# Kernel optimization log

Hardware: AMD Instinct MI355X
Metric: run time of the kernel (lower is better)

The kernel has to match this reference:

```python
import jax, jax.numpy as jnp
import numpy as np

N = 50000      # nodes
E = 800000     # edges
F = 500        # num_features
HID = 64       # hidden_channels
H = 4          # num_heads
HC = HID // H  # headc = 16
C = 8          # num_classes
KHOP = 2       # K hops
CST = 1e-5


def setup_inputs() -> dict:
    key = jax.random.key(0)
    ks = jax.random.split(key, 12)
    s = 0.02
    return {
        "node_feat": jax.random.normal(ks[0], (N, F), dtype=jnp.float32),
        "edge_index": jax.random.randint(ks[1], (2, E), 0, N, dtype=jnp.int64),
        "Wi": jax.random.normal(ks[2], (F, HID), dtype=jnp.float32) * s,
        "bi": jnp.zeros((HID,), dtype=jnp.float32),
        "Wq": jax.random.normal(ks[3], (HID, H * HC), dtype=jnp.float32) * s,
        "bq": jnp.zeros((H * HC,), dtype=jnp.float32),
        "Wk": jax.random.normal(ks[4], (HID, H * HC), dtype=jnp.float32) * s,
        "bk": jnp.zeros((H * HC,), dtype=jnp.float32),
        "Wv": jax.random.normal(ks[5], (HID, H * C), dtype=jnp.float32) * s,
        "bv": jnp.zeros((H * C,), dtype=jnp.float32),
        "Wo": jax.random.normal(ks[6], (H * C, C), dtype=jnp.float32) * s,
        "bo": jnp.zeros((C,), dtype=jnp.float32),
        "hopwise": jnp.ones((KHOP + 1,), dtype=jnp.float32),
        "headwise": jnp.zeros((H, KHOP), dtype=jnp.float32),
        "teleport": jnp.ones((1,), dtype=jnp.float32),
    }


def reference(node_feat, edge_index, Wi, bi, Wq, bq, Wk, bk, Wv, bv, Wo, bo,
              hopwise, headwise, teleport):
    row, col = edge_index[0], edge_index[1]
    # degree(col): in-degree; norm = deg^-1 indexed at row (as in the torch code)
    deg = jax.ops.segment_sum(jnp.ones((E,), dtype=node_feat.dtype), col,
                              num_segments=N)
    deg_inv = jnp.where(deg > 0, 1.0 / deg, 0.0)  # [N]

    x = jax.nn.relu(node_feat @ Wi + bi)          # dropout p=0.0 / eval -> identity
    Q = (1.0 + jax.nn.elu(x @ Wq + bq)).reshape(N, H, HC)
    Kf = (1.0 + jax.nn.elu(x @ Wk + bk)).reshape(N, H, HC)
    V = (x @ Wv + bv).reshape(N, H, C)

    M = jnp.einsum('nhi,nhj->nhij', Kf, V)        # [N,H,HC,C]
    hidden = V * hopwise[0]                       # ind_gamma & gamma_softmax
    layerwise = jax.nn.softmax(headwise, axis=0)  # softmax over heads (dim=-2)

    # global attention (teleport) term
    teleportM = jnp.sum(M, axis=0, keepdims=True) / N      # [1,H,HC,C]
    teleportK = jnp.sum(Kf, axis=0, keepdims=True) / N     # [1,H,HC]
    teleportH = jnp.einsum('nhi,bhij->nhj', Q, teleportM)  # [N,H,C]
    teleportC = jnp.einsum('nhi,bhi->nh', Q, teleportK)[..., None] + CST
    teleportH = (teleportH / teleportC).sum(axis=-2)       # [N,C]

    for hop in range(KHOP):
        # norm[e] = deg_inv[row[e]]  =>  pre-scale source nodes, then scatter-add
        M = jax.ops.segment_sum((M * deg_inv[:, None, None, None])[row], col,
                                num_segments=N)
        Kf = jax.ops.segment_sum((Kf * deg_inv[:, None, None])[row], col,
                                 num_segments=N)
        Hh = jnp.einsum('nhi,nhij->nhj', Q, M)             # [N,H,C]
        Cc = jnp.einsum('nhi,nhi->nh', Q, Kf)[..., None] + CST
        gamma = hopwise[hop + 1] * layerwise[:, hop][:, None]  # [H,1]
        hidden = hidden + gamma * (Hh / Cc)

    # multi_concat output projection
    hidden = hidden.reshape(N, H * C) @ Wo + bo
    return hidden + teleport * teleportH
```

## Files before the change

kernel.cpp:

```cpp
#include <hip/hip_runtime.h>
#include <hip/hip_bf16.h>
#include <stdint.h>
#include <stddef.h>

#define NN 50000
#define NE 800000
#define FIN 500
#define HIDN 64
#define NH 4
#define HCD 16
#define NC 8
#define KVROW 192
#define SROW 576
#define CSTF 1e-5f
#define SCAN_NB 196
#define XBLKS 3125

typedef float f32x2 __attribute__((ext_vector_type(2)));
typedef __attribute__((ext_vector_type(8))) short bf16x8;
typedef __attribute__((ext_vector_type(4))) float f32x4;

__device__ inline float bf_lo(unsigned u) {
    union { unsigned i; float f; } v; v.i = u << 16; return v.f;
}
__device__ inline f32x2 bfpair(unsigned u) {
    union { unsigned i; float f; } lo, hi;
    lo.i = u << 16; hi.i = u & 0xffff0000u;
    f32x2 r; r.x = lo.f; r.y = hi.f; return r;
}
__device__ inline unsigned short f2bf(float f) {
    union { float f; unsigned i; } v; v.f = f;
    unsigned r = v.i + 0x7fffu + ((v.i >> 16) & 1u);
    return (unsigned short)(r >> 16);
}
__device__ inline unsigned pack2bf(float a, float b) {
    __hip_bfloat162 h = __float22bfloat162_rn(make_float2(a, b));
    unsigned r; __builtin_memcpy(&r, &h, 4); return r;
}


__global__ void k_deg_wt(const int* __restrict__ col, int* __restrict__ deg,
                         const float* __restrict__ Wi, unsigned short* __restrict__ Wt) {
    int e = blockIdx.x * blockDim.x + threadIdx.x;
    if (e < NE) atomicAdd(&deg[col[e]], 1);
    if (e < 64 * 512) {
        int c = e >> 9;
        int k = e & 511;
        Wt[e] = (k < FIN) ? f2bf(Wi[(size_t)k * 64 + c]) : (unsigned short)0;
    }
}


__global__ void k_bsum(const int* __restrict__ deg, int* __restrict__ bsum,
                       float* __restrict__ dinv, int* __restrict__ cursor,
                       float* __restrict__ tMK) {
    __shared__ int red[256];
    int b = blockIdx.x, t = threadIdx.x;
    int i = b * 256 + t;
    int d = (i < NN) ? deg[i] : 0;
    if (i < NN) {
        dinv[i] = d > 0 ? 1.0f / (float)d : 0.0f;
        cursor[i] = 0;
    }
    if (b == 0)
        for (int j = t; j < 576; j += 256) tMK[j] = 0.f;
    red[t] = d;
    __syncthreads();
    for (int s = 128; s > 0; s >>= 1) {
        if (t < s) red[t] += red[t + s];
        __syncthreads();
    }
    if (t == 0) bsum[b] = red[0];
}

__global__ void k_bscan(const int* __restrict__ bsum, int* __restrict__ bex) {
    __shared__ int s[256];
    int t = threadIdx.x;
    int own = (t < SCAN_NB) ? bsum[t] : 0;
    s[t] = own;
    __syncthreads();
    for (int d = 1; d < 256; d <<= 1) {
        int v = (t >= d) ? s[t - d] : 0;
        __syncthreads();
        s[t] += v;
        __syncthreads();
    }
    if (t < SCAN_NB) bex[t] = s[t] - own;
}

__global__ void k_expand(const int* __restrict__ deg, const int* __restrict__ bex,
                         int* __restrict__ offs) {
    __shared__ int s[256];
    int b = blockIdx.x, t = threadIdx.x;
    int i = b * 256 + t;
    int v = (i < NN) ? deg[i] : 0;
    s[t] = v;
    __syncthreads();
    for (int d = 1; d < 256; d <<= 1) {
        int a = (t >= d) ? s[t - d] : 0;
        __syncthreads();
        s[t] += a;
        __syncthreads();
    }
    int excl = s[t] - v + bex[b];
    if (i < NN) offs[i] = excl;
    if (i == NN - 1) offs[NN] = excl + v;
}

__global__ void k_scatter(const int* __restrict__ row, const int* __restrict__ col,
                          const int* __restrict__ offs, int* __restrict__ cursor,
                          int* __restrict__ csr_src) {
    int e = blockIdx.x * blockDim.x + threadIdx.x;
    if (e < NE) {
        int c = col[e];
        int pos = offs[c] + atomicAdd(&cursor[c], 1);
        csr_src[pos] = row[e];
    }
}


__global__ __launch_bounds__(256) void k_xgemm(const float* __restrict__ nf,
                                               const unsigned short* __restrict__ Wt,
                                               const float* __restrict__ bi,
                                               float* __restrict__ x) {
    __shared__ float red[4][16][68];
    int t = threadIdx.x;
    int lane = t & 63;
    int w = t >> 6;
    int quad = lane >> 4;
    int l15 = lane & 15;
    int n0 = blockIdx.x * 16;
    const float* rp = nf + (size_t)(n0 + l15) * FIN;
    int kbase = w * 128;

    float4 a0[4], a1[4];
#pragma unroll
    for (int ks = 0; ks < 4; ks++) {
        int kk = kbase + ks * 32 + quad * 8;
        int c0 = kk > 496 ? 496 : kk;
        int c1 = kk + 4 > 496 ? 496 : kk + 4;
        a0[ks] = *(const float4*)(rp + c0);
        a1[ks] = *(const float4*)(rp + c1);
    }

    f32x4 acc[4];
#pragma unroll
    for (int ct = 0; ct < 4; ct++) acc[ct] = (f32x4){0.f, 0.f, 0.f, 0.f};

#pragma unroll
    for (int ks = 0; ks < 4; ks++) {
        union { unsigned u[4]; bf16x8 v; } A;
        A.u[0] = pack2bf(a0[ks].x, a0[ks].y);
        A.u[1] = pack2bf(a0[ks].z, a0[ks].w);
        A.u[2] = pack2bf(a1[ks].x, a1[ks].y);
        A.u[3] = pack2bf(a1[ks].z, a1[ks].w);
        int kk = kbase + ks * 32 + quad * 8;
#pragma unroll
        for (int ct = 0; ct < 4; ct++) {
            bf16x8 b = *(const bf16x8*)&Wt[(size_t)(ct * 16 + l15) * 512 + kk];
            acc[ct] = __builtin_amdgcn_mfma_f32_16x16x32_bf16(A.v, b, acc[ct], 0, 0, 0);
        }
    }

#pragma unroll
    for (int ct = 0; ct < 4; ct++)
#pragma unroll
        for (int r = 0; r < 4; r++)
            red[w][quad * 4 + r][ct * 16 + l15] = acc[ct][r];
    __syncthreads();

    int ocol = t & 63;
    int orow0 = t >> 6;
    float bv = bi[ocol];
#pragma unroll
    for (int i = 0; i < 4; i++) {
        int orow = i * 4 + orow0;
        float s = red[0][orow][ocol] + red[1][orow][ocol]
                + red[2][orow][ocol] + red[3][orow][ocol];
        x[(size_t)(n0 + orow) * 64 + ocol] = fmaxf(s + bv, 0.f);
    }
}


__global__ __launch_bounds__(256) void k_qkv(const float* __restrict__ x,
    const float* __restrict__ Wq, const float* __restrict__ bq,
    const float* __restrict__ Wk, const float* __restrict__ bk,
    const float* __restrict__ Wv, const float* __restrict__ bv,
    const float* __restrict__ hopwise, const float* __restrict__ dinv,
    float* __restrict__ Qg, float* __restrict__ hid,
    unsigned char* __restrict__ kv0, float* __restrict__ tMK) {
    __shared__ float wq_s[64 * 64], wk_s[64 * 64], wv_s[64 * 32];
    __shared__ float bq_s[64], bk_s[64], bv_s[32];
    __shared__ float xs[4][8][64];
    __shared__ float tacc[576];
    int t = threadIdx.x;
    for (int i = t; i < 4096; i += 256) { wq_s[i] = Wq[i]; wk_s[i] = Wk[i]; }
    for (int i = t; i < 2048; i += 256) wv_s[i] = Wv[i];
    if (t < 64) { bq_s[t] = bq[t]; bk_s[t] = bk[t]; }
    if (t >= 64 && t < 96) bv_s[t - 64] = bv[t - 64];
    for (int i = t; i < 576; i += 256) tacc[i] = 0.f;
    __syncthreads();
    int lane = t & 63;
    int w = t >> 6;
    int h = lane >> 4;
    int vcol = lane & 31;
    float hw0 = hopwise[0];
    float tkp = 0.f;
    float tmp_[8];
#pragma unroll
    for (int j = 0; j < 8; j++) tmp_[j] = 0.f;
    int tiles = (NN + 31) >> 5;
    for (int tile = blockIdx.x; tile < tiles; tile += gridDim.x) {
        int n0 = tile * 32 + w * 8;
        __syncthreads();
#pragma unroll
        for (int u = 0; u < 8; u++) {
            int n = n0 + u;
            xs[w][u][lane] = (n < NN) ? x[(size_t)n * 64 + lane] : 0.f;
        }
        __syncthreads();
        float aq[8], ak[8], av[8];
#pragma unroll
        for (int u = 0; u < 8; u++) { aq[u] = 0.f; ak[u] = 0.f; av[u] = 0.f; }
        for (int f = 0; f < 64; f++) {
            float wqv = wq_s[f * 64 + lane];
            float wkv = wk_s[f * 64 + lane];
            float wvv = wv_s[f * 32 + vcol];
#pragma unroll
            for (int u = 0; u < 8; u++) {
                float xf = xs[w][u][f];
                aq[u] = fmaf(xf, wqv, aq[u]);
                ak[u] = fmaf(xf, wkv, ak[u]);
                av[u] = fmaf(xf, wvv, av[u]);
            }
        }
#pragma unroll
        for (int u = 0; u < 8; u++) {
            int n = n0 + u;
            float q = aq[u] + bq_s[lane];
            float k = ak[u] + bk_s[lane];
            float v = av[u] + bv_s[vcol];
            float Qv = q > 0.f ? 1.f + q : expf(q);
            float Kv = k > 0.f ? 1.f + k : expf(k);
            if (n < NN) {
                Qg[(size_t)n * 64 + lane] = Qv;
                float vj[8];
#pragma unroll
                for (int j = 0; j < 8; j++) vj[j] = __shfl(v, h * 8 + j, 64);
                tkp += Kv;
#pragma unroll
                for (int j = 0; j < 8; j++) tmp_[j] += Kv * vj[j];
                float dv = dinv[n];
                unsigned short* kvrow = (unsigned short*)(kv0 + (size_t)n * KVROW);
                kvrow[lane] = f2bf(Kv * dv);
                if (lane < 32) kvrow[64 + lane] = f2bf(v);
                if (lane < 32) hid[(size_t)n * 32 + lane] = v * hw0;
            }
        }
    }
#pragma unroll
    for (int j = 0; j < 8; j++) atomicAdd(&tacc[lane * 8 + j], tmp_[j]);
    atomicAdd(&tacc[512 + lane], tkp);
    __syncthreads();
    for (int i = t; i < 576; i += 256) atomicAdd(&tMK[i], tacc[i]);
}


__global__ __launch_bounds__(256) void k_hop0(const unsigned char* __restrict__ kv0,
    const int* __restrict__ offs, const int* __restrict__ csr_src,
    const float* __restrict__ dinv, const float* __restrict__ Qg,
    const float* __restrict__ hopwise, const float* __restrict__ headwise,
    unsigned char* __restrict__ S1, float* __restrict__ hid) {
    int t = threadIdx.x;
    int lane = t & 63;
    int n = __builtin_amdgcn_readfirstlane((blockIdx.x * 256 + t) >> 6);
    if (n >= NN) return;
    int h = lane >> 4;
    float e0 = expf(headwise[0]);
    float e1 = expf(headwise[2]);
    float e2 = expf(headwise[4]);
    float e3 = expf(headwise[6]);
    float esum = e0 + e1 + e2 + e3;
    float eh = (h == 0) ? e0 : ((h == 1) ? e1 : ((h == 2) ? e2 : e3));
    float gam = hopwise[1] * eh / esum;

    int hoff = 128 + h * 16;
    int o0 = offs[n], o1 = offs[n + 1];
    float qv = Qg[(size_t)n * 64 + lane];
    float kacc = 0.f;
    f32x2 A0 = {0.f, 0.f}, A1 = {0.f, 0.f}, B0 = {0.f, 0.f}, B1 = {0.f, 0.f};

    int idx[8];
#pragma unroll
    for (int q = 0; q < 8; q++) idx[q] = (o0 + q < o1) ? csr_src[o0 + q] : NN;
    for (int e = o0; e < o1; e += 8) {
        float kk_[8]; uint4 vv[8];
#pragma unroll
        for (int q = 0; q < 8; q++) {
            const unsigned char* r = kv0 + (size_t)idx[q] * KVROW;
            kk_[q] = bf_lo(((const unsigned short*)r)[lane]);
            vv[q] = *(const uint4*)(r + hoff);
        }
        int e2n = e + 8;
#pragma unroll
        for (int q = 0; q < 8; q++) idx[q] = (e2n + q < o1) ? csr_src[e2n + q] : NN;
#pragma unroll
        for (int q = 0; q < 8; q++) {
            float ka = kk_[q];
            f32x2 ka2; ka2.x = ka; ka2.y = ka;
            kacc += ka;
            A0 += ka2 * bfpair(vv[q].x);
            A1 += ka2 * bfpair(vv[q].y);
            B0 += ka2 * bfpair(vv[q].z);
            B1 += ka2 * bfpair(vv[q].w);
        }
    }
    {
        float dv = dinv[n];
        float s8 = dv * 8.f;
        float s16 = dv * 16.f;
        unsigned char* drow = S1 + (size_t)n * SROW;
        unsigned kb8 = __builtin_amdgcn_cvt_pk_fp8_f32(kacc * s8, 0.f, 0, false);
        drow[lane] = (unsigned char)(kb8 & 0xff);
        unsigned u0 = __builtin_amdgcn_cvt_pk_fp8_f32(A0.x * s16, A0.y * s16, 0, false);
        u0 = __builtin_amdgcn_cvt_pk_fp8_f32(A1.x * s16, A1.y * s16, u0, true);
        unsigned u1 = __builtin_amdgcn_cvt_pk_fp8_f32(B0.x * s16, B0.y * s16, 0, false);
        u1 = __builtin_amdgcn_cvt_pk_fp8_f32(B1.x * s16, B1.y * s16, u1, true);
        uint2 pv; pv.x = u0; pv.y = u1;
        *(uint2*)(drow + 64 + lane * 8) = pv;
    }
    float hh[8];
    hh[0] = qv * A0.x; hh[1] = qv * A0.y; hh[2] = qv * A1.x; hh[3] = qv * A1.y;
    hh[4] = qv * B0.x; hh[5] = qv * B0.y; hh[6] = qv * B1.x; hh[7] = qv * B1.y;
    float cc = qv * kacc;
#pragma unroll
    for (int s = 1; s < 16; s <<= 1) {
#pragma unroll
        for (int j = 0; j < 8; j++) hh[j] += __shfl_xor(hh[j], s, 16);
        cc += __shfl_xor(cc, s, 16);
    }
    if ((lane & 15) < 8) {
        int j = lane & 7;
        float val = j < 4 ? (j < 2 ? (j == 0 ? hh[0] : hh[1]) : (j == 2 ? hh[2] : hh[3]))
                          : (j < 6 ? (j == 4 ? hh[4] : hh[5]) : (j == 6 ? hh[6] : hh[7]));
        size_t idx2 = (size_t)n * 32 + h * 8 + j;
        hid[idx2] += gam * val / (cc + CSTF);
    }
}


__global__ __launch_bounds__(256) void k_prop1(const unsigned char* __restrict__ Sold,
    const int* __restrict__ offs, const int* __restrict__ csr_src,
    const float* __restrict__ Qg, const float* __restrict__ hopwise,
    const float* __restrict__ headwise, float* __restrict__ hid) {
    int t = threadIdx.x;
    int lane = t & 63;
    int n = __builtin_amdgcn_readfirstlane((blockIdx.x * 256 + t) >> 6);
    if (n >= NN) return;
    int h = lane >> 4;
    float e0 = expf(headwise[1]);
    float e1 = expf(headwise[3]);
    float e2 = expf(headwise[5]);
    float e3 = expf(headwise[7]);
    float esum = e0 + e1 + e2 + e3;
    float eh = (h == 0) ? e0 : ((h == 1) ? e1 : ((h == 2) ? e2 : e3));
    float gam = hopwise[2] * eh / esum * 0.0625f;

    int o0 = offs[n], o1 = offs[n + 1];
    float qv = Qg[(size_t)n * 64 + lane];
    float kacc = 0.f;
    f32x2 A0 = {0.f, 0.f}, A1 = {0.f, 0.f}, B0 = {0.f, 0.f}, B1 = {0.f, 0.f};

    int idx[8];
#pragma unroll
    for (int q = 0; q < 8; q++) idx[q] = (o0 + q < o1) ? csr_src[o0 + q] : NN;
    for (int e = o0; e < o1; e += 8) {
        unsigned kb[8]; uint2 mv[8];
#pragma unroll
        for (int q = 0; q < 8; q++) {
            const unsigned char* r = Sold + (size_t)idx[q] * SROW;
            kb[q] = r[lane];
            mv[q] = *(const uint2*)(r + 64 + lane * 8);
        }
        int e2n = e + 8;
#pragma unroll
        for (int q = 0; q < 8; q++) idx[q] = (e2n + q < o1) ? csr_src[e2n + q] : NN;
#pragma unroll
        for (int q = 0; q < 8; q++) {
            f32x2 kv = __builtin_amdgcn_cvt_pk_f32_fp8(kb[q], false);
            kacc += kv.x;
            A0 += __builtin_amdgcn_cvt_pk_f32_fp8(mv[q].x, false);
            A1 += __builtin_amdgcn_cvt_pk_f32_fp8(mv[q].x, true);
            B0 += __builtin_amdgcn_cvt_pk_f32_fp8(mv[q].y, false);
            B1 += __builtin_amdgcn_cvt_pk_f32_fp8(mv[q].y, true);
        }
    }
    kacc *= 0.125f;
    float hh[8];
    hh[0] = qv * A0.x; hh[1] = qv * A0.y; hh[2] = qv * A1.x; hh[3] = qv * A1.y;
    hh[4] = qv * B0.x; hh[5] = qv * B0.y; hh[6] = qv * B1.x; hh[7] = qv * B1.y;
    float cc = qv * kacc;
#pragma unroll
    for (int s = 1; s < 16; s <<= 1) {
#pragma unroll
        for (int j = 0; j < 8; j++) hh[j] += __shfl_xor(hh[j], s, 16);
        cc += __shfl_xor(cc, s, 16);
    }
    if ((lane & 15) < 8) {
        int j = lane & 7;
        float val = j < 4 ? (j < 2 ? (j == 0 ? hh[0] : hh[1]) : (j == 2 ? hh[2] : hh[3]))
                          : (j < 6 ? (j == 4 ? hh[4] : hh[5]) : (j == 6 ? hh[6] : hh[7]));
        size_t idx2 = (size_t)n * 32 + h * 8 + j;
        hid[idx2] += gam * val / (cc + CSTF);
    }
}


__global__ __launch_bounds__(256) void k_final(const float* __restrict__ hid,
    const float* __restrict__ Qg, const float* __restrict__ Wo,
    const float* __restrict__ bo, const float* __restrict__ tMK,
    const float* __restrict__ teleport, float* __restrict__ out) {
    __shared__ float tm[512];
    __shared__ float tk[64];
    __shared__ float wo[256];
    __shared__ float bos[8];
    int t = threadIdx.x;
    const float invN = 1.0f / (float)NN;
    for (int i = t; i < 512; i += 256) tm[i] = tMK[i] * invN;
    if (t < 64) tk[t] = tMK[512 + t] * invN;
    wo[t] = Wo[t & 255];
    if (t < 8) bos[t] = bo[t];
    __syncthreads();
    float tp = teleport[0];
    int lane = t & 63;
    int sub = lane & 7;
    int g = lane >> 3;
    int wid = (blockIdx.x * 256 + t) >> 6;
    int nwaves = gridDim.x * 4;
    for (int nb = wid * 8; nb < NN; nb += nwaves * 8) {
        int n = nb + g;
        if (n < NN) {
            const float* hrow = hid + (size_t)n * 32;
            const float* qrow = Qg + (size_t)n * 64;
            float o = bos[sub];
#pragma unroll
            for (int m = 0; m < 32; m++) o = fmaf(hrow[m], wo[m * 8 + sub], o);
            float th = 0.f;
#pragma unroll
            for (int h2 = 0; h2 < 4; h2++) {
                float num = 0.f, den = 0.f;
#pragma unroll
                for (int i = 0; i < 16; i++) {
                    float q = qrow[h2 * 16 + i];
                    num = fmaf(q, tm[h2 * 128 + i * 8 + sub], num);
                    den = fmaf(q, tk[h2 * 16 + i], den);
                }
                th += num / (den + CSTF);
            }
            out[(size_t)n * 8 + sub] = o + tp * th;
        }
    }
}


extern "C" void kernel_launch(void* const* d_in, const int* in_sizes, int n_in,
                              void* d_out, int out_size, void* d_ws, size_t ws_size,
                              hipStream_t stream) {
    const float* nf = (const float*)d_in[0];
    const int* ei = (const int*)d_in[1];
    const float* Wi = (const float*)d_in[2];
    const float* bi = (const float*)d_in[3];
    const float* Wq = (const float*)d_in[4];
    const float* bq = (const float*)d_in[5];
    const float* Wk = (const float*)d_in[6];
    const float* bk = (const float*)d_in[7];
    const float* Wv = (const float*)d_in[8];
    const float* bv = (const float*)d_in[9];
    const float* Wo = (const float*)d_in[10];
    const float* bo = (const float*)d_in[11];
    const float* hopwise = (const float*)d_in[12];
    const float* headwise = (const float*)d_in[13];
    const float* teleport = (const float*)d_in[14];
    float* out = (float*)d_out;

    char* base = (char*)d_ws;
    size_t off = 0;
    auto alloc = [&](size_t bytes) -> void* {
        void* p = base + off;
        off = (off + bytes + 255) & ~(size_t)255;
        return p;
    };
    int* deg = (int*)alloc(NN * 4);
    int* cursor = (int*)alloc(NN * 4);
    int* offs = (int*)alloc((NN + 1) * 4);
    int* bsum = (int*)alloc(256 * 4);
    int* bex = (int*)alloc(256 * 4);
    float* dinv = (float*)alloc(NN * 4);
    int* csr_src = (int*)alloc((size_t)NE * 4);
    unsigned short* Wt = (unsigned short*)alloc(64 * 512 * 2);
    float* xbuf = (float*)alloc((size_t)NN * 64 * 4);
    float* Qg = (float*)alloc((size_t)NN * 64 * 4);
    float* hid = (float*)alloc((size_t)NN * 32 * 4);
    unsigned char* kv0 = (unsigned char*)alloc((size_t)(NN + 1) * KVROW);
    unsigned char* S1 = (unsigned char*)alloc((size_t)(NN + 1) * SROW);
    float* tMK = (float*)alloc(576 * 4);

    const int* rowp = ei;
    const int* colp = ei + NE;

    hipMemsetAsync(deg, 0, NN * 4, stream);
    hipMemsetAsync(kv0 + (size_t)NN * KVROW, 0, KVROW, stream);
    hipMemsetAsync(S1 + (size_t)NN * SROW, 0, SROW, stream);

    k_deg_wt<<<(NE + 255) / 256, 256, 0, stream>>>(colp, deg, Wi, Wt);
    k_bsum<<<SCAN_NB, 256, 0, stream>>>(deg, bsum, dinv, cursor, tMK);
    k_bscan<<<1, 256, 0, stream>>>(bsum, bex);
    k_expand<<<SCAN_NB, 256, 0, stream>>>(deg, bex, offs);
    k_scatter<<<(NE + 255) / 256, 256, 0, stream>>>(rowp, colp, offs, cursor, csr_src);
    k_xgemm<<<XBLKS, 256, 0, stream>>>(nf, Wt, bi, xbuf);
    k_qkv<<<768, 256, 0, stream>>>(xbuf, Wq, bq, Wk, bk, Wv, bv, hopwise, dinv,
                                   Qg, hid, kv0, tMK);
    k_hop0<<<(NN * 64 + 255) / 256, 256, 0, stream>>>(kv0, offs, csr_src, dinv, Qg,
                                                      hopwise, headwise, S1, hid);
    k_prop1<<<(NN * 64 + 255) / 256, 256, 0, stream>>>(S1, offs, csr_src, Qg,
                                                       hopwise, headwise, hid);
    k_final<<<1563, 256, 0, stream>>>(hid, Qg, Wo, bo, tMK, teleport, out);
}
```

Measured before the change: 458.4 us.

## Split wave into half-waves per edge and realign propagated K/M arrays

Both hop kernels now process two neighbours per wave iteration, one per half-wave. Each lane owns two K channels and accumulates the full 2x8 KV outer-product slice for them, and the two halves are combined with a cross-half shuffle. The single 576-byte fp8 S1 row is replaced by separate 512-byte M and 64-byte K arrays, and the kv0 row stride is padded from 192 to 256 bytes. This gives aligned 16-byte loads and stores and halves the number of gather instructions per edge. The cost is extra shuffles and a padded kv0 buffer.

```diff
diff --git a/kernel.cpp b/kernel.cpp
--- a/kernel.cpp
+++ b/kernel.cpp
@@ -10,8 +10,7 @@
 #define NH 4
 #define HCD 16
 #define NC 8
-#define KVROW 192
-#define SROW 576
+#define KVROW 256
 #define CSTF 1e-5f
 #define SCAN_NB 196
 #define XBLKS 3125
@@ -270,12 +269,15 @@
     const int* __restrict__ offs, const int* __restrict__ csr_src,
     const float* __restrict__ dinv, const float* __restrict__ Qg,
     const float* __restrict__ hopwise, const float* __restrict__ headwise,
-    unsigned char* __restrict__ S1, float* __restrict__ hid) {
+    unsigned char* __restrict__ Marr, unsigned char* __restrict__ Karr,
+    float* __restrict__ hid) {
     int t = threadIdx.x;
     int lane = t & 63;
     int n = __builtin_amdgcn_readfirstlane((blockIdx.x * 256 + t) >> 6);
     if (n >= NN) return;
-    int h = lane >> 4;
+    int m = lane & 31;
+    int half = lane >> 5;
+    int h = m >> 3;
     float e0 = expf(headwise[0]);
     float e1 = expf(headwise[2]);
     float e2 = expf(headwise[4]);
@@ -284,72 +286,105 @@
     float eh = (h == 0) ? e0 : ((h == 1) ? e1 : ((h == 2) ? e2 : e3));
     float gam = hopwise[1] * eh / esum;
 
-    int hoff = 128 + h * 16;
     int o0 = offs[n], o1 = offs[n + 1];
-    float qv = Qg[(size_t)n * 64 + lane];
-    float kacc = 0.f;
-    f32x2 A0 = {0.f, 0.f}, A1 = {0.f, 0.f}, B0 = {0.f, 0.f}, B1 = {0.f, 0.f};
+    f32x2 qv2 = *(const f32x2*)(Qg + (size_t)n * 64 + m * 2);
+    f32x2 acc0[4], acc1[4], kacc2;
+#pragma unroll
+    for (int p = 0; p < 4; p++) { acc0[p] = (f32x2){0.f, 0.f}; acc1[p] = (f32x2){0.f, 0.f}; }
+    kacc2 = (f32x2){0.f, 0.f};
 
     int idx[8];
 #pragma unroll
     for (int q = 0; q < 8; q++) idx[q] = (o0 + q < o1) ? csr_src[o0 + q] : NN;
     for (int e = o0; e < o1; e += 8) {
-        float kk_[8]; uint4 vv[8];
-#pragma unroll
-        for (int q = 0; q < 8; q++) {
-            const unsigned char* r = kv0 + (size_t)idx[q] * KVROW;
-            kk_[q] = bf_lo(((const unsigned short*)r)[lane]);
-            vv[q] = *(const uint4*)(r + hoff);
+        unsigned kw[4]; uint4 vv[4];
+#pragma unroll
+        for (int p = 0; p < 4; p++) {
+            int sel = half ? idx[2 * p + 1] : idx[2 * p];
+            const unsigned char* r = kv0 + (size_t)sel * KVROW;
+            kw[p] = *(const unsigned*)(r + m * 4);
+            vv[p] = *(const uint4*)(r + 128 + h * 16);
         }
         int e2n = e + 8;
 #pragma unroll
         for (int q = 0; q < 8; q++) idx[q] = (e2n + q < o1) ? csr_src[e2n + q] : NN;
 #pragma unroll
-        for (int q = 0; q < 8; q++) {
-            float ka = kk_[q];
-            f32x2 ka2; ka2.x = ka; ka2.y = ka;
-            kacc += ka;
-            A0 += ka2 * bfpair(vv[q].x);
-            A1 += ka2 * bfpair(vv[q].y);
-            B0 += ka2 * bfpair(vv[q].z);
-            B1 += ka2 * bfpair(vv[q].w);
-        }
-    }
-    {
-        float dv = dinv[n];
-        float s8 = dv * 8.f;
-        float s16 = dv * 16.f;
-        unsigned char* drow = S1 + (size_t)n * SROW;
-        unsigned kb8 = __builtin_amdgcn_cvt_pk_fp8_f32(kacc * s8, 0.f, 0, false);
-        drow[lane] = (unsigned char)(kb8 & 0xff);
-        unsigned u0 = __builtin_amdgcn_cvt_pk_fp8_f32(A0.x * s16, A0.y * s16, 0, false);
-        u0 = __builtin_amdgcn_cvt_pk_fp8_f32(A1.x * s16, A1.y * s16, u0, true);
-        unsigned u1 = __builtin_amdgcn_cvt_pk_fp8_f32(B0.x * s16, B0.y * s16, 0, false);
-        u1 = __builtin_amdgcn_cvt_pk_fp8_f32(B1.x * s16, B1.y * s16, u1, true);
-        uint2 pv; pv.x = u0; pv.y = u1;
-        *(uint2*)(drow + 64 + lane * 8) = pv;
-    }
-    float hh[8];
-    hh[0] = qv * A0.x; hh[1] = qv * A0.y; hh[2] = qv * A1.x; hh[3] = qv * A1.y;
-    hh[4] = qv * B0.x; hh[5] = qv * B0.y; hh[6] = qv * B1.x; hh[7] = qv * B1.y;
-    float cc = qv * kacc;
-#pragma unroll
-    for (int s = 1; s < 16; s <<= 1) {
-#pragma unroll
-        for (int j = 0; j < 8; j++) hh[j] += __shfl_xor(hh[j], s, 16);
-        cc += __shfl_xor(cc, s, 16);
-    }
-    if ((lane & 15) < 8) {
-        int j = lane & 7;
-        float val = j < 4 ? (j < 2 ? (j == 0 ? hh[0] : hh[1]) : (j == 2 ? hh[2] : hh[3]))
-                          : (j < 6 ? (j == 4 ? hh[4] : hh[5]) : (j == 6 ? hh[6] : hh[7]));
-        size_t idx2 = (size_t)n * 32 + h * 8 + j;
-        hid[idx2] += gam * val / (cc + CSTF);
-    }
-}
-
-
-__global__ __launch_bounds__(256) void k_prop1(const unsigned char* __restrict__ Sold,
+        for (int p = 0; p < 4; p++) {
+            f32x2 kf = bfpair(kw[p]);
+            f32x2 v01 = bfpair(vv[p].x);
+            f32x2 v23 = bfpair(vv[p].y);
+            f32x2 v45 = bfpair(vv[p].z);
+            f32x2 v67 = bfpair(vv[p].w);
+            f32x2 k0; k0.x = kf.x; k0.y = kf.x;
+            f32x2 k1; k1.x = kf.y; k1.y = kf.y;
+            acc0[0] += k0 * v01; acc0[1] += k0 * v23;
+            acc0[2] += k0 * v45; acc0[3] += k0 * v67;
+            acc1[0] += k1 * v01; acc1[1] += k1 * v23;
+            acc1[2] += k1 * v45; acc1[3] += k1 * v67;
+            kacc2 += kf;
+        }
+    }
+#pragma unroll
+    for (int p = 0; p < 4; p++) {
+        acc0[p].x += __shfl_xor(acc0[p].x, 32, 64);
+        acc0[p].y += __shfl_xor(acc0[p].y, 32, 64);
+        acc1[p].x += __shfl_xor(acc1[p].x, 32, 64);
+        acc1[p].y += __shfl_xor(acc1[p].y, 32, 64);
+    }
+    kacc2.x += __shfl_xor(kacc2.x, 32, 64);
+    kacc2.y += __shfl_xor(kacc2.y, 32, 64);
+
+    float dv = dinv[n];
+    float s8 = dv * 8.f;
+    float s16 = dv * 16.f;
+    if (half == 0) {
+        uint4 pk;
+        unsigned u;
+        u = __builtin_amdgcn_cvt_pk_fp8_f32(acc0[0].x * s16, acc0[0].y * s16, 0, false);
+        u = __builtin_amdgcn_cvt_pk_fp8_f32(acc0[1].x * s16, acc0[1].y * s16, u, true);
+        pk.x = u;
+        u = __builtin_amdgcn_cvt_pk_fp8_f32(acc0[2].x * s16, acc0[2].y * s16, 0, false);
+        u = __builtin_amdgcn_cvt_pk_fp8_f32(acc0[3].x * s16, acc0[3].y * s16, u, true);
+        pk.y = u;
+        u = __builtin_amdgcn_cvt_pk_fp8_f32(acc1[0].x * s16, acc1[0].y * s16, 0, false);
+        u = __builtin_amdgcn_cvt_pk_fp8_f32(acc1[1].x * s16, acc1[1].y * s16, u, true);
+        pk.z = u;
+        u = __builtin_amdgcn_cvt_pk_fp8_f32(acc1[2].x * s16, acc1[2].y * s16, 0, false);
+        u = __builtin_amdgcn_cvt_pk_fp8_f32(acc1[3].x * s16, acc1[3].y * s16, u, true);
+        pk.w = u;
+        *(uint4*)(Marr + (size_t)n * 512 + m * 16) = pk;
+        unsigned kb = __builtin_amdgcn_cvt_pk_fp8_f32(kacc2.x * s8, kacc2.y * s8, 0, false);
+        *(unsigned short*)(Karr + (size_t)n * 64 + m * 2) = (unsigned short)(kb & 0xffff);
+    }
+
+    f32x2 qx; qx.x = qv2.x; qx.y = qv2.x;
+    f32x2 qy; qy.x = qv2.y; qy.y = qv2.y;
+    f32x2 hh[4];
+#pragma unroll
+    for (int p = 0; p < 4; p++) hh[p] = qx * acc0[p] + qy * acc1[p];
+    float cc = qv2.x * kacc2.x + qv2.y * kacc2.y;
+#pragma unroll
+    for (int s = 1; s < 8; s <<= 1) {
+#pragma unroll
+        for (int p = 0; p < 4; p++) {
+            hh[p].x += __shfl_xor(hh[p].x, s, 64);
+            hh[p].y += __shfl_xor(hh[p].y, s, 64);
+        }
+        cc += __shfl_xor(cc, s, 64);
+    }
+    if (half == 0) {
+        int j = m & 7;
+        float val = (j < 4) ? ((j < 2) ? ((j == 0) ? hh[0].x : hh[0].y)
+                                       : ((j == 2) ? hh[1].x : hh[1].y))
+                            : ((j < 6) ? ((j == 4) ? hh[2].x : hh[2].y)
+                                       : ((j == 6) ? hh[3].x : hh[3].y));
+        hid[(size_t)n * 32 + m] += gam * val / (cc + CSTF);
+    }
+}
+
+
+__global__ __launch_bounds__(256) void k_prop1(const unsigned char* __restrict__ Marr,
+    const unsigned char* __restrict__ Karr,
     const int* __restrict__ offs, const int* __restrict__ csr_src,
     const float* __restrict__ Qg, const float* __restrict__ hopwise,
     const float* __restrict__ headwise, float* __restrict__ hid) {
@@ -357,7 +392,9 @@
     int lane = t & 63;
     int n = __builtin_amdgcn_readfirstlane((blockIdx.x * 256 + t) >> 6);
     if (n >= NN) return;
-    int h = lane >> 4;
+    int m = lane & 31;
+    int half = lane >> 5;
+    int h = m >> 3;
     float e0 = expf(headwise[1]);
     float e1 = expf(headwise[3]);
     float e2 = expf(headwise[5]);
@@ -367,51 +404,67 @@
     float gam = hopwise[2] * eh / esum * 0.0625f;
 
     int o0 = offs[n], o1 = offs[n + 1];
-    float qv = Qg[(size_t)n * 64 + lane];
-    float kacc = 0.f;
-    f32x2 A0 = {0.f, 0.f}, A1 = {0.f, 0.f}, B0 = {0.f, 0.f}, B1 = {0.f, 0.f};
+    f32x2 qv2 = *(const f32x2*)(Qg + (size_t)n * 64 + m * 2);
+    f32x2 acc0[4], acc1[4], kacc2;
+#pragma unroll
+    for (int p = 0; p < 4; p++) { acc0[p] = (f32x2){0.f, 0.f}; acc1[p] = (f32x2){0.f, 0.f}; }
+    kacc2 = (f32x2){0.f, 0.f};
 
     int idx[8];
 #pragma unroll
     for (int q = 0; q < 8; q++) idx[q] = (o0 + q < o1) ? csr_src[o0 + q] : NN;
     for (int e = o0; e < o1; e += 8) {
-        unsigned kb[8]; uint2 mv[8];
-#pragma unroll
-        for (int q = 0; q < 8; q++) {
-            const unsigned char* r = Sold + (size_t)idx[q] * SROW;
-            kb[q] = r[lane];
-            mv[q] = *(const uint2*)(r + 64 + lane * 8);
+        uint4 mv[4]; unsigned kb[4];
+#pragma unroll
+        for (int p = 0; p < 4; p++) {
+            int sel = half ? idx[2 * p + 1] : idx[2 * p];
+            mv[p] = *(const uint4*)(Marr + (size_t)sel * 512 + m * 16);
+            kb[p] = *(const unsigned short*)(Karr + (size_t)sel * 64 + m * 2);
         }
         int e2n = e + 8;
 #pragma unroll
         for (int q = 0; q < 8; q++) idx[q] = (e2n + q < o1) ? csr_src[e2n + q] : NN;
 #pragma unroll
-        for (int q = 0; q < 8; q++) {
-            f32x2 kv = __builtin_amdgcn_cvt_pk_f32_fp8(kb[q], false);
-            kacc += kv.x;
-            A0 += __builtin_amdgcn_cvt_pk_f32_fp8(mv[q].x, false);
-            A1 += __builtin_amdgcn_cvt_pk_f32_fp8(mv[q].x, true);
-            B0 += __builtin_amdgcn_cvt_pk_f32_fp8(mv[q].y, false);
-            B1 += __builtin_amdgcn_cvt_pk_f32_fp8(mv[q].y, true);
-        }
-    }
-    kacc *= 0.125f;
-    float hh[8];
-    hh[0] = qv * A0.x; hh[1] = qv * A0.y; hh[2] = qv * A1.x; hh[3] = qv * A1.y;
-    hh[4] = qv * B0.x; hh[5] = qv * B0.y; hh[6] = qv * B1.x; hh[7] = qv * B1.y;
-    float cc = qv * kacc;
-#pragma unroll
-    for (int s = 1; s < 16; s <<= 1) {
-#pragma unroll
-        for (int j = 0; j < 8; j++) hh[j] += __shfl_xor(hh[j], s, 16);
-        cc += __shfl_xor(cc, s, 16);
-    }
-    if ((lane & 15) < 8) {
-        int j = lane & 7;
-        float val = j < 4 ? (j < 2 ? (j == 0 ? hh[0] : hh[1]) : (j == 2 ? hh[2] : hh[3]))
-                          : (j < 6 ? (j == 4 ? hh[4] : hh[5]) : (j == 6 ? hh[6] : hh[7]));
-        size_t idx2 = (size_t)n * 32 + h * 8 + j;
-        hid[idx2] += gam * val / (cc + CSTF);
+        for (int p = 0; p < 4; p++) {
+            acc0[0] += __builtin_amdgcn_cvt_pk_f32_fp8(mv[p].x, false);
+            acc0[1] += __builtin_amdgcn_cvt_pk_f32_fp8(mv[p].x, true);
+            acc0[2] += __builtin_amdgcn_cvt_pk_f32_fp8(mv[p].y, false);
+            acc0[3] += __builtin_amdgcn_cvt_pk_f32_fp8(mv[p].y, true);
+            acc1[0] += __builtin_amdgcn_cvt_pk_f32_fp8(mv[p].z, false);
+            acc1[1] += __builtin_amdgcn_cvt_pk_f32_fp8(mv[p].z, true);
+            acc1[2] += __builtin_amdgcn_cvt_pk_f32_fp8(mv[p].w, false);
+            acc1[3] += __builtin_amdgcn_cvt_pk_f32_fp8(mv[p].w, true);
+            kacc2 += __builtin_amdgcn_cvt_pk_f32_fp8(kb[p], false);
+        }
+    }
+    f32x2 qx; qx.x = qv2.x; qx.y = qv2.x;
+    f32x2 qy; qy.x = qv2.y; qy.y = qv2.y;
+    f32x2 hh[4];
+#pragma unroll
+    for (int p = 0; p < 4; p++) hh[p] = qx * acc0[p] + qy * acc1[p];
+    float cc = (qv2.x * kacc2.x + qv2.y * kacc2.y) * 0.125f;
+#pragma unroll
+    for (int s = 1; s < 8; s <<= 1) {
+#pragma unroll
+        for (int p = 0; p < 4; p++) {
+            hh[p].x += __shfl_xor(hh[p].x, s, 64);
+            hh[p].y += __shfl_xor(hh[p].y, s, 64);
+        }
+        cc += __shfl_xor(cc, s, 64);
+    }
+#pragma unroll
+    for (int p = 0; p < 4; p++) {
+        hh[p].x += __shfl_xor(hh[p].x, 32, 64);
+        hh[p].y += __shfl_xor(hh[p].y, 32, 64);
+    }
+    cc += __shfl_xor(cc, 32, 64);
+    if (half == 0) {
+        int j = m & 7;
+        float val = (j < 4) ? ((j < 2) ? ((j == 0) ? hh[0].x : hh[0].y)
+                                       : ((j == 2) ? hh[1].x : hh[1].y))
+                            : ((j < 6) ? ((j == 4) ? hh[2].x : hh[2].y)
+                                       : ((j == 6) ? hh[3].x : hh[3].y));
+        hid[(size_t)n * 32 + m] += gam * val / (cc + CSTF);
     }
 }
 
@@ -502,7 +555,8 @@
     float* Qg = (float*)alloc((size_t)NN * 64 * 4);
     float* hid = (float*)alloc((size_t)NN * 32 * 4);
     unsigned char* kv0 = (unsigned char*)alloc((size_t)(NN + 1) * KVROW);
-    unsigned char* S1 = (unsigned char*)alloc((size_t)(NN + 1) * SROW);
+    unsigned char* Marr = (unsigned char*)alloc((size_t)(NN + 1) * 512);
+    unsigned char* Karr = (unsigned char*)alloc((size_t)(NN + 1) * 64);
     float* tMK = (float*)alloc(576 * 4);
 
     const int* rowp = ei;
@@ -510,7 +564,8 @@
 
     hipMemsetAsync(deg, 0, NN * 4, stream);
     hipMemsetAsync(kv0 + (size_t)NN * KVROW, 0, KVROW, stream);
-    hipMemsetAsync(S1 + (size_t)NN * SROW, 0, SROW, stream);
+    hipMemsetAsync(Marr + (size_t)NN * 512, 0, 512, stream);
+    hipMemsetAsync(Karr + (size_t)NN * 64, 0, 64, stream);
 
     k_deg_wt<<<(NE + 255) / 256, 256, 0, stream>>>(colp, deg, Wi, Wt);
     k_bsum<<<SCAN_NB, 256, 0, stream>>>(deg, bsum, dinv, cursor, tMK);
@@ -521,8 +576,8 @@
     k_qkv<<<768, 256, 0, stream>>>(xbuf, Wq, bq, Wk, bk, Wv, bv, hopwise, dinv,
                                    Qg, hid, kv0, tMK);
     k_hop0<<<(NN * 64 + 255) / 256, 256, 0, stream>>>(kv0, offs, csr_src, dinv, Qg,
-                                                      hopwise, headwise, S1, hid);
-    k_prop1<<<(NN * 64 + 255) / 256, 256, 0, stream>>>(S1, offs, csr_src, Qg,
+                                                      hopwise, headwise, Marr, Karr, hid);
+    k_prop1<<<(NN * 64 + 255) / 256, 256, 0, stream>>>(Marr, Karr, offs, csr_src, Qg,
                                                        hopwise, headwise, hid);
     k_final<<<1563, 256, 0, stream>>>(hid, Qg, Wo, bo, tMK, teleport, out);
 }
```

New measurement: 520.2 us. 1.13x slower.
